# Performance work log

Hardware: AMD Instinct MI355X
Metric: run time of the kernel (lower is better)

## Reference

```python
import jax, jax.numpy as jnp
import numpy as np

H, W = 512, 512
N_GAUSS = 4096
T_EPS = 1e-3          # early-termination threshold from the torch loop
COV_DIAG = 25.0       # hardcoded cov_2d = eye(2) * 25 in rasterize_gaussians


def quat_to_rot(q):
    # standard (w, x, y, z) quaternion -> rotation matrix, with normalization
    q = q / jnp.linalg.norm(q)
    w, x, y, z = q[0], q[1], q[2], q[3]
    return jnp.array([
        [1 - 2 * (y * y + z * z), 2 * (x * y - w * z),     2 * (x * z + w * y)],
        [2 * (x * y + w * z),     1 - 2 * (x * x + z * z), 2 * (y * z - w * x)],
        [2 * (x * z - w * y),     2 * (y * z + w * x),     1 - 2 * (x * x + y * y)],
    ])


def setup_inputs() -> dict:
    key = jax.random.key(0)
    k0, k1, k2, k3 = jax.random.split(key, 4)
    xy = jax.random.uniform(k0, (N_GAUSS, 2), minval=-2.0, maxval=2.0)
    z = jax.random.uniform(k1, (N_GAUSS, 1), minval=4.0, maxval=10.0)
    positions = jnp.concatenate([xy, z], axis=-1)                    # [N,3], z>0
    colors = jax.random.uniform(k2, (N_GAUSS, 3))                    # [N,3] in [0,1]
    opacities = jax.random.uniform(k3, (N_GAUSS,)) * 0.5             # [N]
    quaternion = jnp.array([1.0, 0.05, 0.02, 0.01], dtype=jnp.float32)
    cam_position = jnp.zeros(3, dtype=jnp.float32)
    intrinsics = jnp.array([[500.0, 0.0, 256.0],
                            [0.0, 500.0, 256.0],
                            [0.0, 0.0, 1.0]], dtype=jnp.float32)
    background_color = jnp.zeros(3, dtype=jnp.float32)
    return {"positions": positions, "colors": colors, "opacities": opacities,
            "quaternion": quaternion, "cam_position": cam_position,
            "intrinsics": intrinsics, "background_color": background_color}


def _render(positions, colors, opacities, quaternion, cam_position, intrinsics,
            background_color):
    R = quat_to_rot(quaternion)                                      # [3,3]
    pos_cam = (positions - cam_position[None, :]) @ R.T              # [N,3]
    proj = pos_cam @ intrinsics.T                                    # [N,3]
    screen = proj[:, :2] / proj[:, 2:3]                              # [N,2]
    depths = proj[:, 2]                                              # [N]

    order = jnp.argsort(-depths)                                     # back-to-front
    centers_s = screen[order]
    colors_s = colors[order]
    opac_s = opacities[order]
    depth_s = pos_cam[order, 2]

    yy, xx = jnp.meshgrid(jnp.arange(H, dtype=jnp.float32),
                          jnp.arange(W, dtype=jnp.float32), indexing="ij")
    pix = jnp.stack([xx, yy], axis=-1)                               # [H,W,2] (x,y)

    init_color = jnp.broadcast_to(background_color[:, None, None], (3, H, W))
    carry0 = (init_color, jnp.zeros((H, W)), jnp.zeros((H, W)), jnp.ones((H, W)))

    def step(carry, g):
        color_acc, depth_acc, alpha_acc, T = carry
        center, color, opacity, depth = g
        # emulate the `if transmittance.max() < 1e-3: break` exactly: once T
        # saturates it is monotone, so masking all later contributions == break
        active = (jnp.max(T) >= T_EPS).astype(T.dtype)
        diff = pix - center[None, None, :]                           # [H,W,2]
        mahal = jnp.sum(diff * diff, axis=-1) / COV_DIAG             # cov_inv = I/25
        alpha = jnp.clip(jnp.exp(-0.5 * mahal) * opacity, 0.0, 1.0) * active
        ta = T * alpha
        color_acc = color_acc + ta[None, :, :] * color[:, None, None]
        depth_acc = depth_acc + ta * depth
        alpha_acc = alpha_acc + ta
        T = T * (1.0 - alpha)
        return (color_acc, depth_acc, alpha_acc, T), None

    (image, depth_map, alpha_map, _), _ = jax.lax.scan(
        step, carry0, (centers_s, colors_s, opac_s, depth_s))
    return image, depth_map, alpha_map


def reference(positions, colors, opacities, quaternion, cam_position, intrinsics,
              background_color):
    return _render(positions, colors, opacities, quaternion, cam_position,
                   intrinsics, background_color)
```

## Files before the change

kernel.cpp:

```cpp
#include <hip/hip_runtime.h>
#include <hip/hip_bf16.h>

#define N_GAUSS 4096
#define H 512
#define W 512
#define HW (H * W)

#define SEG 4
#define GSEG (N_GAUSS / SEG)
#define CULL2 1444.0f
#define CAPS 256


__device__ __forceinline__ float depth_key(const float* __restrict__ pos,
                                           float r20, float r21, float r22,
                                           float c0, float c1, float c2, int g) {
    float px = pos[3 * g] - c0, py = pos[3 * g + 1] - c1, pz = pos[3 * g + 2] - c2;
    return -(r20 * px + r21 * py + r22 * pz);
}

__global__ __launch_bounds__(256) void rank_partial_kernel(
        const float* __restrict__ pos, const float* __restrict__ quat,
        const float* __restrict__ cam, int* __restrict__ rankpart) {
    __shared__ __align__(16) float skj[256];
    __shared__ float ski[256];
    int t = threadIdx.x;
    int bi = blockIdx.x & 15, bj = blockIdx.x >> 4;
    float qw = quat[0], qx = quat[1], qy = quat[2], qz = quat[3];
    float qn = 1.0f / sqrtf(qw * qw + qx * qx + qy * qy + qz * qz);
    qw *= qn; qx *= qn; qy *= qn; qz *= qn;
    float r20 = 2.f * (qx * qz - qw * qy), r21 = 2.f * (qy * qz + qw * qx),
          r22 = 1.f - 2.f * (qx * qx + qy * qy);
    float c0 = cam[0], c1 = cam[1], c2 = cam[2];
    int gi = bi * 256 + t, gj = bj * 256 + t;
    ski[t] = depth_key(pos, r20, r21, r22, c0, c1, c2, gi);
    skj[t] = depth_key(pos, r20, r21, r22, c0, c1, c2, gj);
    __syncthreads();
    float ki = ski[t];
    int jbase = bj * 256;
    int r = 0;
    #pragma unroll
    for (int j = 0; j < 256; j += 4) {
        float4 k4 = *reinterpret_cast<const float4*>(&skj[j]);
        r += (k4.x < ki) || (k4.x == ki && (jbase + j + 0) < gi);
        r += (k4.y < ki) || (k4.y == ki && (jbase + j + 1) < gi);
        r += (k4.z < ki) || (k4.z == ki && (jbase + j + 2) < gi);
        r += (k4.w < ki) || (k4.w == ki && (jbase + j + 3) < gi);
    }
    rankpart[bj * N_GAUSS + gi] = r;
}

__global__ __launch_bounds__(256) void scatter_kernel(
        const float* __restrict__ pos, const float* __restrict__ quat,
        const float* __restrict__ cam, const float* __restrict__ Km,
        const float* __restrict__ colors, const float* __restrict__ opac,
        const int* __restrict__ rankpart,
        float4* __restrict__ sorted, float2* __restrict__ cxy) {
    int t = threadIdx.x;
    int i = blockIdx.x * 256 + t;
    int r = 0;
    #pragma unroll
    for (int b = 0; b < 16; ++b) r += rankpart[b * N_GAUSS + i];
    float qw = quat[0], qx = quat[1], qy = quat[2], qz = quat[3];
    float qn = 1.0f / sqrtf(qw * qw + qx * qx + qy * qy + qz * qz);
    qw *= qn; qx *= qn; qy *= qn; qz *= qn;
    float r00 = 1.f - 2.f * (qy * qy + qz * qz), r01 = 2.f * (qx * qy - qw * qz), r02 = 2.f * (qx * qz + qw * qy);
    float r10 = 2.f * (qx * qy + qw * qz), r11 = 1.f - 2.f * (qx * qx + qz * qz), r12 = 2.f * (qy * qz - qw * qx);
    float r20 = 2.f * (qx * qz - qw * qy), r21 = 2.f * (qy * qz + qw * qx), r22 = 1.f - 2.f * (qx * qx + qy * qy);
    float px = pos[3 * i] - cam[0], py = pos[3 * i + 1] - cam[1], pz = pos[3 * i + 2] - cam[2];
    float X = r00 * px + r01 * py + r02 * pz;
    float Y = r10 * px + r11 * py + r12 * pz;
    float Z = r20 * px + r21 * py + r22 * pz;
    float u = Km[0] * X + Km[1] * Y + Km[2] * Z;
    float v = Km[3] * X + Km[4] * Y + Km[5] * Z;
    float w = Km[6] * X + Km[7] * Y + Km[8] * Z;
    float sx = u / w, sy = v / w;
    sorted[2 * r]     = make_float4(sx, sy, Z, opac[i]);
    sorted[2 * r + 1] = make_float4(colors[3 * i], colors[3 * i + 1], colors[3 * i + 2], 0.f);
    cxy[r] = make_float2(sx, sy);
}

__global__ __launch_bounds__(1024, 8) void render_fused_kernel(
        const float4* __restrict__ gs, const float2* __restrict__ cxy,
        const float* __restrict__ bg, float* __restrict__ out) {
    __shared__ unsigned long long smask[64];
    __shared__ int sprefix[SEG][17];
    __shared__ unsigned short sidx[N_GAUSS];
    __shared__ __align__(16) float4 cmp[SEG][2 * CAPS];
    __shared__ float comb[SEG][6][256];
    __shared__ int stmax;

    int tid = threadIdx.x;
    int lane = tid & 63;
    int wave = tid >> 6;
    int seg = wave >> 2;
    int lw = wave & 3;
    int p = tid & 255;
    int tile = (blockIdx.x * 341) & 1023;
    int tx0 = (tile & 31) * 16, ty0 = (tile >> 5) * 16;
    float px = (float)(tx0 + (p & 15)), py = (float)(ty0 + (p >> 4));
    float tcx = tx0 + 7.5f, tcy = ty0 + 7.5f;

    if (tid == 0) stmax = 0;

    for (int k = 0; k < 4; ++k) {
        int sc = seg * 16 + lw * 4 + k;
        int g = sc * 64 + lane;
        float2 c2 = cxy[g];
        float ddx = c2.x - tcx, ddy = c2.y - tcy;
        bool pred = (ddx * ddx + ddy * ddy <= CULL2);
        unsigned long long m = __ballot(pred ? 1 : 0);
        if (pred) {
            int pos = __popcll(m & ((1ull << lane) - 1ull));
            sidx[sc * 64 + pos] = (unsigned short)g;
        }
        if (lane == 0) smask[sc] = m;
    }
    __syncthreads();

    if (lw == 0 && lane < 16) {
        int c = __popcll(smask[seg * 16 + lane]);
        int inc = c;
        #pragma unroll
        for (int d = 1; d < 16; d <<= 1) {
            int n = __shfl_up(inc, d, 64);
            if (lane >= d) inc += n;
        }
        sprefix[seg][lane] = inc - c;
        if (lane == 15) {
            sprefix[seg][16] = inc;
            atomicMax(&stmax, inc);
        }
    }
    __syncthreads();
    int total = sprefix[seg][16];
    int tmax = stmax;

    float T = 1.f, cr = 0.f, cg = 0.f, cb = 0.f, da = 0.f, aa = 0.f;

    for (int base = 0; base < tmax; base += CAPS) {
        int cnt = min(CAPS, total - base);
        for (int s = p; s < cnt; s += 256) {
            int gpos = base + s;
            int lo = 0, hi = 16;
            #pragma unroll
            for (int it = 0; it < 4; ++it) {
                int mid = (lo + hi) >> 1;
                if (sprefix[seg][mid] <= gpos) lo = mid; else hi = mid;
            }
            int idx = sidx[(seg * 16 + lo) * 64 + (gpos - sprefix[seg][lo])];
            cmp[seg][2 * s]     = gs[2 * idx];
            cmp[seg][2 * s + 1] = gs[2 * idx + 1];
        }
        __syncthreads();
        #pragma unroll 2
        for (int g = 0; g < cnt; ++g) {
            float4 GA = cmp[seg][2 * g];
            float dx = px - GA.x, dy = py - GA.y;
            float al = __expf(-0.02f * (dx * dx + dy * dy)) * GA.w;
            float ta = T * al;
            float4 GC = cmp[seg][2 * g + 1];
            cr += ta * GC.x; cg += ta * GC.y; cb += ta * GC.z;
            da += ta * GA.z; aa += ta;
            T -= ta;
        }
        __syncthreads();
    }

    comb[seg][0][p] = cr;  comb[seg][1][p] = cg;  comb[seg][2][p] = cb;
    comb[seg][3][p] = da;  comb[seg][4][p] = aa;  comb[seg][5][p] = T;
    __syncthreads();
    if (seg == 0) {
        float r = 0.f, g2 = 0.f, b = 0.f, d = 0.f, a = 0.f;
        #pragma unroll
        for (int s = SEG - 1; s >= 0; --s) {
            float Ts = comb[s][5][p];
            r  = comb[s][0][p] + Ts * r;
            g2 = comb[s][1][p] + Ts * g2;
            b  = comb[s][2][p] + Ts * b;
            d  = comb[s][3][p] + Ts * d;
            a  = comb[s][4][p] + Ts * a;
        }
        int pid = (ty0 + (p >> 4)) * W + tx0 + (p & 15);
        out[pid]          = bg[0] + r;
        out[HW + pid]     = bg[1] + g2;
        out[2 * HW + pid] = bg[2] + b;
        out[3 * HW + pid] = d;
        out[4 * HW + pid] = a;
    }
}

extern "C" void kernel_launch(void* const* d_in, const int* in_sizes, int n_in,
                              void* d_out, int out_size, void* d_ws, size_t ws_size,
                              hipStream_t stream) {
    const float* positions = (const float*)d_in[0];
    const float* colors    = (const float*)d_in[1];
    const float* opacities = (const float*)d_in[2];
    const float* quat      = (const float*)d_in[3];
    const float* cam       = (const float*)d_in[4];
    const float* intr      = (const float*)d_in[5];
    const float* bg        = (const float*)d_in[6];
    float* out = (float*)d_out;

    float*  ws       = (float*)d_ws;
    float4* sorted   = (float4*)ws;
    float2* cxy      = (float2*)(ws + 32768);
    int*    rankpart = (int*)(ws + 49152);

    rank_partial_kernel<<<dim3(256), dim3(256), 0, stream>>>(
        positions, quat, cam, rankpart);
    scatter_kernel<<<dim3(16), dim3(256), 0, stream>>>(
        positions, quat, cam, intr, colors, opacities, rankpart,
        sorted, cxy);
    render_fused_kernel<<<dim3(1024), dim3(1024), 0, stream>>>(
        sorted, cxy, bg, out);
}
```

Baseline: 110.5 us.

## Fuse projection, per-tile depth sort and rendering into one kernel

Removes the global rank and scatter kernels. Each tile block now projects all Gaussians itself, culls them against the tile, and sorts only the surviving subset by depth with a local rank sort in shared memory. Rendering then splits that sorted list evenly across the four segments, with no chunked refill loop. This cuts two launches and global round trips, but every block repeats the projection of all 4096 Gaussians. The culled list is capped at MAXS=1024 entries, and any overflow beyond that is silently dropped.

```diff
diff --git a/kernel.cpp b/kernel.cpp
--- a/kernel.cpp
+++ b/kernel.cpp
@@ -5,166 +5,118 @@
 #define H 512
 #define W 512
 #define HW (H * W)
+#define SEG 4
+#define CULL2 1444.0f
+#define MAXS 1024
 
-#define SEG 4
-#define GSEG (N_GAUSS / SEG)
-#define CULL2 1444.0f
-#define CAPS 256
+__global__ __launch_bounds__(1024, 8) void render_all_kernel(
+        const float* __restrict__ pos, const float* __restrict__ colors,
+        const float* __restrict__ opac, const float* __restrict__ quat,
+        const float* __restrict__ cam, const float* __restrict__ Km,
+        const float* __restrict__ bg, float* __restrict__ out) {
+    __shared__ __align__(16) float skey[MAXS + 4];
+    __shared__ __align__(16) unsigned short sidxs[MAXS + 4];
+    __shared__ __align__(16) float2 scxy[MAXS];
+    __shared__ __align__(16) float4 scmp[MAXS];
+    __shared__ __align__(16) float4 scol[MAXS];
+    __shared__ float comb[SEG][6][256];
+    __shared__ int scnt;
 
+    int tid = threadIdx.x;
+    int lane = tid & 63;
+    int wave = tid >> 6;
+    int seg = wave >> 2;
+    int p = tid & 255;
+    int tile = (blockIdx.x * 341) & 1023;
+    int tx0 = (tile & 31) * 16, ty0 = (tile >> 5) * 16;
+    float px = (float)(tx0 + (p & 15)), py = (float)(ty0 + (p >> 4));
+    float tcx = tx0 + 7.5f, tcy = ty0 + 7.5f;
 
-__device__ __forceinline__ float depth_key(const float* __restrict__ pos,
-                                           float r20, float r21, float r22,
-                                           float c0, float c1, float c2, int g) {
-    float px = pos[3 * g] - c0, py = pos[3 * g + 1] - c1, pz = pos[3 * g + 2] - c2;
-    return -(r20 * px + r21 * py + r22 * pz);
-}
+    if (tid == 0) scnt = 0;
 
-__global__ __launch_bounds__(256) void rank_partial_kernel(
-        const float* __restrict__ pos, const float* __restrict__ quat,
-        const float* __restrict__ cam, int* __restrict__ rankpart) {
-    __shared__ __align__(16) float skj[256];
-    __shared__ float ski[256];
-    int t = threadIdx.x;
-    int bi = blockIdx.x & 15, bj = blockIdx.x >> 4;
-    float qw = quat[0], qx = quat[1], qy = quat[2], qz = quat[3];
-    float qn = 1.0f / sqrtf(qw * qw + qx * qx + qy * qy + qz * qz);
-    qw *= qn; qx *= qn; qy *= qn; qz *= qn;
-    float r20 = 2.f * (qx * qz - qw * qy), r21 = 2.f * (qy * qz + qw * qx),
-          r22 = 1.f - 2.f * (qx * qx + qy * qy);
-    float c0 = cam[0], c1 = cam[1], c2 = cam[2];
-    int gi = bi * 256 + t, gj = bj * 256 + t;
-    ski[t] = depth_key(pos, r20, r21, r22, c0, c1, c2, gi);
-    skj[t] = depth_key(pos, r20, r21, r22, c0, c1, c2, gj);
-    __syncthreads();
-    float ki = ski[t];
-    int jbase = bj * 256;
-    int r = 0;
-    #pragma unroll
-    for (int j = 0; j < 256; j += 4) {
-        float4 k4 = *reinterpret_cast<const float4*>(&skj[j]);
-        r += (k4.x < ki) || (k4.x == ki && (jbase + j + 0) < gi);
-        r += (k4.y < ki) || (k4.y == ki && (jbase + j + 1) < gi);
-        r += (k4.z < ki) || (k4.z == ki && (jbase + j + 2) < gi);
-        r += (k4.w < ki) || (k4.w == ki && (jbase + j + 3) < gi);
-    }
-    rankpart[bj * N_GAUSS + gi] = r;
-}
-
-__global__ __launch_bounds__(256) void scatter_kernel(
-        const float* __restrict__ pos, const float* __restrict__ quat,
-        const float* __restrict__ cam, const float* __restrict__ Km,
-        const float* __restrict__ colors, const float* __restrict__ opac,
-        const int* __restrict__ rankpart,
-        float4* __restrict__ sorted, float2* __restrict__ cxy) {
-    int t = threadIdx.x;
-    int i = blockIdx.x * 256 + t;
-    int r = 0;
-    #pragma unroll
-    for (int b = 0; b < 16; ++b) r += rankpart[b * N_GAUSS + i];
     float qw = quat[0], qx = quat[1], qy = quat[2], qz = quat[3];
     float qn = 1.0f / sqrtf(qw * qw + qx * qx + qy * qy + qz * qz);
     qw *= qn; qx *= qn; qy *= qn; qz *= qn;
     float r00 = 1.f - 2.f * (qy * qy + qz * qz), r01 = 2.f * (qx * qy - qw * qz), r02 = 2.f * (qx * qz + qw * qy);
     float r10 = 2.f * (qx * qy + qw * qz), r11 = 1.f - 2.f * (qx * qx + qz * qz), r12 = 2.f * (qy * qz - qw * qx);
     float r20 = 2.f * (qx * qz - qw * qy), r21 = 2.f * (qy * qz + qw * qx), r22 = 1.f - 2.f * (qx * qx + qy * qy);
-    float px = pos[3 * i] - cam[0], py = pos[3 * i + 1] - cam[1], pz = pos[3 * i + 2] - cam[2];
-    float X = r00 * px + r01 * py + r02 * pz;
-    float Y = r10 * px + r11 * py + r12 * pz;
-    float Z = r20 * px + r21 * py + r22 * pz;
-    float u = Km[0] * X + Km[1] * Y + Km[2] * Z;
-    float v = Km[3] * X + Km[4] * Y + Km[5] * Z;
-    float w = Km[6] * X + Km[7] * Y + Km[8] * Z;
-    float sx = u / w, sy = v / w;
-    sorted[2 * r]     = make_float4(sx, sy, Z, opac[i]);
-    sorted[2 * r + 1] = make_float4(colors[3 * i], colors[3 * i + 1], colors[3 * i + 2], 0.f);
-    cxy[r] = make_float2(sx, sy);
-}
+    float c0 = cam[0], c1 = cam[1], c2 = cam[2];
+    float k0 = Km[0], k1 = Km[1], k2 = Km[2];
+    float k3 = Km[3], k4 = Km[4], k5 = Km[5];
+    float k6 = Km[6], k7 = Km[7], k8 = Km[8];
 
-__global__ __launch_bounds__(1024, 8) void render_fused_kernel(
-        const float4* __restrict__ gs, const float2* __restrict__ cxy,
-        const float* __restrict__ bg, float* __restrict__ out) {
-    __shared__ unsigned long long smask[64];
-    __shared__ int sprefix[SEG][17];
-    __shared__ unsigned short sidx[N_GAUSS];
-    __shared__ __align__(16) float4 cmp[SEG][2 * CAPS];
-    __shared__ float comb[SEG][6][256];
-    __shared__ int stmax;
+    __syncthreads();
 
-    int tid = threadIdx.x;
-    int lane = tid & 63;
-    int wave = tid >> 6;
-    int seg = wave >> 2;
-    int lw = wave & 3;
-    int p = tid & 255;
-    int tile = (blockIdx.x * 341) & 1023;
-    int tx0 = (tile & 31) * 16, ty0 = (tile >> 5) * 16;
-    float px = (float)(tx0 + (p & 15)), py = (float)(ty0 + (p >> 4));
-    float tcx = tx0 + 7.5f, tcy = ty0 + 7.5f;
+    const float4* p4 = reinterpret_cast<const float4*>(pos);
+    float4 pva = p4[3 * tid], pvb = p4[3 * tid + 1], pvc = p4[3 * tid + 2];
+    float gxa[4] = {pva.x, pva.w, pvb.z, pvc.y};
+    float gya[4] = {pva.y, pvb.x, pvb.w, pvc.z};
+    float gza[4] = {pva.z, pvb.y, pvc.x, pvc.w};
 
-    if (tid == 0) stmax = 0;
-
+    #pragma unroll
     for (int k = 0; k < 4; ++k) {
-        int sc = seg * 16 + lw * 4 + k;
-        int g = sc * 64 + lane;
-        float2 c2 = cxy[g];
-        float ddx = c2.x - tcx, ddy = c2.y - tcy;
+        int g = tid * 4 + k;
+        float ax = gxa[k] - c0, ay = gya[k] - c1, az = gza[k] - c2;
+        float X = r00 * ax + r01 * ay + r02 * az;
+        float Y = r10 * ax + r11 * ay + r12 * az;
+        float Z = r20 * ax + r21 * ay + r22 * az;
+        float u = k0 * X + k1 * Y + k2 * Z;
+        float v = k3 * X + k4 * Y + k5 * Z;
+        float w = k6 * X + k7 * Y + k8 * Z;
+        float sx = u / w, sy = v / w;
+        float ddx = sx - tcx, ddy = sy - tcy;
         bool pred = (ddx * ddx + ddy * ddy <= CULL2);
         unsigned long long m = __ballot(pred ? 1 : 0);
+        int base = 0;
+        if (lane == 0) base = atomicAdd(&scnt, __popcll(m));
+        base = __shfl(base, 0);
         if (pred) {
-            int pos = __popcll(m & ((1ull << lane) - 1ull));
-            sidx[sc * 64 + pos] = (unsigned short)g;
+            int slot = base + __popcll(m & ((1ull << lane) - 1ull));
+            if (slot < MAXS) {
+                skey[slot] = Z;
+                sidxs[slot] = (unsigned short)g;
+                scxy[slot] = make_float2(sx, sy);
+            }
         }
-        if (lane == 0) smask[sc] = m;
+    }
+    __syncthreads();
+    int n = min(scnt, MAXS);
+    if (tid < 4) { skey[n + tid] = -1e30f; sidxs[n + tid] = 0; }
+    __syncthreads();
+
+    if (tid < n) {
+        float Zi = skey[tid];
+        int idxi = sidxs[tid];
+        int pad4 = (n + 3) & ~3;
+        int r = 0;
+        for (int j = 0; j < pad4; j += 4) {
+            float4 kz = *reinterpret_cast<const float4*>(&skey[j]);
+            ushort4 si = *reinterpret_cast<const ushort4*>(&sidxs[j]);
+            r += (kz.x > Zi) || (kz.x == Zi && (int)si.x < idxi);
+            r += (kz.y > Zi) || (kz.y == Zi && (int)si.y < idxi);
+            r += (kz.z > Zi) || (kz.z == Zi && (int)si.z < idxi);
+            r += (kz.w > Zi) || (kz.w == Zi && (int)si.w < idxi);
+        }
+        float2 xy = scxy[tid];
+        scmp[r] = make_float4(xy.x, xy.y, Zi, opac[idxi]);
+        scol[r] = make_float4(colors[3 * idxi], colors[3 * idxi + 1],
+                              colors[3 * idxi + 2], 0.f);
     }
     __syncthreads();
 
-    if (lw == 0 && lane < 16) {
-        int c = __popcll(smask[seg * 16 + lane]);
-        int inc = c;
-        #pragma unroll
-        for (int d = 1; d < 16; d <<= 1) {
-            int n = __shfl_up(inc, d, 64);
-            if (lane >= d) inc += n;
-        }
-        sprefix[seg][lane] = inc - c;
-        if (lane == 15) {
-            sprefix[seg][16] = inc;
-            atomicMax(&stmax, inc);
-        }
-    }
-    __syncthreads();
-    int total = sprefix[seg][16];
-    int tmax = stmax;
-
+    int q = (n + 3) >> 2;
+    int beg = min(seg * q, n), end = min(beg + q, n);
     float T = 1.f, cr = 0.f, cg = 0.f, cb = 0.f, da = 0.f, aa = 0.f;
-
-    for (int base = 0; base < tmax; base += CAPS) {
-        int cnt = min(CAPS, total - base);
-        for (int s = p; s < cnt; s += 256) {
-            int gpos = base + s;
-            int lo = 0, hi = 16;
-            #pragma unroll
-            for (int it = 0; it < 4; ++it) {
-                int mid = (lo + hi) >> 1;
-                if (sprefix[seg][mid] <= gpos) lo = mid; else hi = mid;
-            }
-            int idx = sidx[(seg * 16 + lo) * 64 + (gpos - sprefix[seg][lo])];
-            cmp[seg][2 * s]     = gs[2 * idx];
-            cmp[seg][2 * s + 1] = gs[2 * idx + 1];
-        }
-        __syncthreads();
-        #pragma unroll 2
-        for (int g = 0; g < cnt; ++g) {
-            float4 GA = cmp[seg][2 * g];
-            float dx = px - GA.x, dy = py - GA.y;
-            float al = __expf(-0.02f * (dx * dx + dy * dy)) * GA.w;
-            float ta = T * al;
-            float4 GC = cmp[seg][2 * g + 1];
-            cr += ta * GC.x; cg += ta * GC.y; cb += ta * GC.z;
-            da += ta * GA.z; aa += ta;
-            T -= ta;
-        }
-        __syncthreads();
+    #pragma unroll 2
+    for (int g = beg; g < end; ++g) {
+        float4 GA = scmp[g];
+        float dx = px - GA.x, dy = py - GA.y;
+        float al = __expf(-0.02f * (dx * dx + dy * dy)) * GA.w;
+        float ta = T * al;
+        float4 GC = scol[g];
+        cr += ta * GC.x; cg += ta * GC.y; cb += ta * GC.z;
+        da += ta * GA.z; aa += ta;
+        T -= ta;
     }
 
     comb[seg][0][p] = cr;  comb[seg][1][p] = cg;  comb[seg][2][p] = cb;
@@ -201,17 +153,8 @@
     const float* intr      = (const float*)d_in[5];
     const float* bg        = (const float*)d_in[6];
     float* out = (float*)d_out;
+    (void)d_ws; (void)ws_size;
 
-    float*  ws       = (float*)d_ws;
-    float4* sorted   = (float4*)ws;
-    float2* cxy      = (float2*)(ws + 32768);
-    int*    rankpart = (int*)(ws + 49152);
-
-    rank_partial_kernel<<<dim3(256), dim3(256), 0, stream>>>(
-        positions, quat, cam, rankpart);
-    scatter_kernel<<<dim3(16), dim3(256), 0, stream>>>(
-        positions, quat, cam, intr, colors, opacities, rankpart,
-        sorted, cxy);
-    render_fused_kernel<<<dim3(1024), dim3(1024), 0, stream>>>(
-        sorted, cxy, bg, out);
+    render_all_kernel<<<dim3(1024), dim3(1024), 0, stream>>>(
+        positions, colors, opacities, quat, cam, intr, bg, out);
 }
```

After: 106.5 us. 1.04x faster.
